# Optimization experiments

Hardware: AMD Instinct MI355X
Metric: run time of the kernel (lower is better)

The kernel has to match this reference:

```python
import jax, jax.numpy as jnp
import numpy as np

N_WIRES = 6
DIM = 1 << N_WIRES  # 64, equals input channel dim C for amplitude encoding
HID = N_WIRES       # hidden_dim = len(ops)


def _rx(theta):
    c = jnp.cos(theta / 2).astype(jnp.complex64)
    s = jnp.sin(theta / 2).astype(jnp.complex64)
    return jnp.stack([jnp.stack([c, -1j * s]), jnp.stack([-1j * s, c])])


def _ry(theta):
    c = jnp.cos(theta / 2).astype(jnp.complex64)
    s = jnp.sin(theta / 2).astype(jnp.complex64)
    return jnp.stack([jnp.stack([c, -s]), jnp.stack([s, c])])


def _apply_1q(state, U, wire):
    # state: (N, 2, 2, ..., 2); apply 2x2 U on qubit axis wire+1
    s = jnp.moveaxis(state, wire + 1, 1)
    s = jnp.einsum('ab,nb...->na...', U, s)
    return jnp.moveaxis(s, 1, wire + 1)


def _apply_cnot(state, c, t):
    # flip target axis where control bit == 1
    s = jnp.moveaxis(state, (c + 1, t + 1), (1, 2))
    s = jnp.concatenate([s[:, :1], jnp.flip(s[:, 1:2], axis=2)], axis=1)
    return jnp.moveaxis(s, (1, 2), (c + 1, t + 1))


def _expval_z(state, wire):
    # <Z_wire> = P(bit=0) - P(bit=1)
    p = state.real ** 2 + state.imag ** 2
    p = jnp.moveaxis(p, wire + 1, 1).reshape(p.shape[0], 2, -1)
    return p[:, 0].sum(-1) - p[:, 1].sum(-1)


def _value_layer(x_flat, params, qk):
    # amplitude encoding: normalize input into state amplitudes (C == DIM)
    norm = jnp.linalg.norm(x_flat, axis=-1, keepdims=True)
    psi = (x_flat / norm).astype(jnp.complex64)
    state = psi.reshape((x_flat.shape[0],) + (2,) * N_WIRES)
    rx0, ry0, ry1 = params[0], params[1], params[2]
    for j in range(N_WIRES):
        state = _apply_1q(state, _rx(rx0[j]), j)
        state = _apply_1q(state, _ry(ry0[j]), j)
    for j in range(N_WIRES):
        state = _apply_cnot(state, j, (j + 1) % N_WIRES)
    for j in range(N_WIRES):
        state = _apply_1q(state, _ry(ry1[j]), j)
    if qk:
        z0 = _expval_z(state, 0)
        return jnp.stack([z0] * HID, axis=-1)  # qk=True replicates wire-0 <Z>
    return jnp.stack([_expval_z(state, w) for w in range(N_WIRES)], axis=-1)


def setup_inputs() -> dict:
    key = jax.random.key(0)
    k1, k2, k3, k4 = jax.random.split(key, 4)
    B, T, C = 16, 2048, DIM
    return {
        'x': jax.random.normal(k1, (B, T, C), dtype=jnp.float32),
        'params_q': jax.random.normal(k2, (3, N_WIRES), dtype=jnp.float32),
        'params_k': jax.random.normal(k3, (3, N_WIRES), dtype=jnp.float32),
        'params_v': jax.random.normal(k4, (3, N_WIRES), dtype=jnp.float32),
    }


def reference(x, params_q, params_k, params_v):
    B, T, C = x.shape
    xf = x.reshape(B * T, C)
    q = _value_layer(xf, params_q, True).reshape(B, T, HID)
    k = _value_layer(xf, params_k, True).reshape(B, T, HID)
    v = _value_layer(xf, params_v, False).reshape(B, T, HID)
    scores = jnp.einsum('btd,bsd->bts', q, k) / jnp.sqrt(jnp.float32(HID))
    attn = jax.nn.softmax(scores, axis=-1)
    return jnp.einsum('bts,bsd->btd', attn, v)
```

## Files before the change

### kernel.cpp

```cpp
#include <hip/hip_runtime.h>
#include <math.h>

#define NWIRES 6
#define DIM 64
#define NTOK 32768
#define NBATCH 16
#define TPB 2048
#define NMOM 16
#define SQRT6F 2.4494897427831781f
#define APAD 76

typedef short bf16x8 __attribute__((ext_vector_type(8)));
typedef float f32x4  __attribute__((ext_vector_type(4)));

__device__ __forceinline__ unsigned f2bfbits(float f) {
    unsigned u = __float_as_uint(f);
    return (u + 0x7FFF + ((u >> 16) & 1)) >> 16;
}
__device__ __forceinline__ float bfbits2f(unsigned b) {
    return __uint_as_float(b << 16);
}

__global__ __launch_bounds__(128) void qsa_build(
        const float* __restrict__ pq,
        const float* __restrict__ pk,
        const float* __restrict__ pv,
        unsigned short* __restrict__ gA) {
    __shared__ float sTc[64], sTs[64], sP[24];
    int circ = blockIdx.x;
    const float* p = (circ == 0) ? pq : (circ == 1 ? pk : pv);
    int tid = threadIdx.x;

    if (tid < 64) {
        int b = tid;
        float d = 0.f;
#pragma unroll
        for (int j = 0; j < 6; ++j)
            d += 0.5f * p[j] * ((b & (32 >> j)) ? -1.f : 1.f);
        float sd, cd;
        sincosf(d, &sd, &cd);
        sTc[b] = cd;
        sTs[b] = sd;
        if (b < 12) {
            float s, cc;
            sincosf(0.5f * p[6 + b], &s, &cc);
            sP[b * 2 + 0] = cc;
            sP[b * 2 + 1] = s;
        }
    }
    __syncthreads();

    int ph = tid >> 6;
    int k  = tid & 63;
    const float* sTx = ph ? sTs : sTc;
    float v[64];
#pragma unroll
    for (int g = 0; g < 64; ++g)
        v[g] = (__popc(g & k) & 1) ? -sTx[g] : sTx[g];

#pragma unroll
    for (int M = 32; M >= 1; M >>= 1) {
#pragma unroll
        for (int i = 0; i < 64; ++i) {
            if (i & M) continue;
            int j = i | M;
            float a = v[i], b = v[j];
            v[i] = a + b; v[j] = a - b;
        }
    }

#pragma unroll
    for (int layer = 0; layer < 2; ++layer) {
        const float* Pl = sP + layer * 12;
#pragma unroll
        for (int w = 0; w < 6; ++w) {
            int M = 32 >> w;
            float c = Pl[w * 2], s = Pl[w * 2 + 1];
#pragma unroll
            for (int i = 0; i < 64; ++i) {
                if (i & M) continue;
                int j = i | M;
                float a = v[i], b = v[j];
                v[i] = c * a - s * b;
                v[j] = s * a + c * b;
            }
        }
        if (layer == 0) {
#pragma unroll
            for (int i = 32; i < 64; ++i) {
                if (i & 16) continue;
                int j = i | 16;
                float t = v[i]; v[i] = v[j]; v[j] = t;
            }
#pragma unroll
            for (int w = 1; w < 5; ++w) {
                int MC = 32 >> w, MT = MC >> 1;
#pragma unroll
                for (int i = 0; i < 64; ++i) {
                    if (!(i & MC) || (i & MT)) continue;
                    int j = i | MT;
                    float t = v[i]; v[i] = v[j]; v[j] = t;
                }
            }
#pragma unroll
            for (int i = 1; i < 32; i += 2) {
                int j = i | 32;
                float t = v[i]; v[i] = v[j]; v[j] = t;
            }
        }
    }

    unsigned short* g0 = gA + (size_t)circ * (2 * 128 * APAD);
#pragma unroll
    for (int i = 0; i < 64; ++i) {
        int row = ph * 64 + i;
        unsigned hb = f2bfbits(v[i]);
        unsigned lb = f2bfbits(v[i] - bfbits2f(hb));
        g0[row * APAD + k] = (unsigned short)hb;
        g0[128 * APAD + row * APAD + k] = (unsigned short)lb;
    }
}

__global__ __attribute__((amdgpu_waves_per_eu(1, 4)))
__launch_bounds__(256) void qsa_sim(
        const float* __restrict__ x,
        const unsigned short* __restrict__ gA,
        float* __restrict__ zq,
        float* __restrict__ kv) {
    __shared__ __align__(16) unsigned short sA[2 * 128 * APAD];
    unsigned short* sAh = sA;
    unsigned short* sAl = sA + 128 * APAD;
    int tid = threadIdx.x;
    int tbase = blockIdx.x * 128;
    int circ = blockIdx.y;

    int lane = tid & 63, wv = tid >> 6;
    int q4 = lane >> 4, c16 = lane & 15;
    int mytok0 = wv * 32 + c16;
    const float* xr0 = x + ((size_t)(tbase + mytok0)) * 64;
    float4 rw[4];
#pragma unroll
    for (int ks = 0; ks < 2; ++ks) {
        rw[ks * 2 + 0] = *(const float4*)(xr0 + ks * 32 + q4 * 8);
        rw[ks * 2 + 1] = *(const float4*)(xr0 + ks * 32 + q4 * 8 + 4);
    }

    {
        const uint4* gsrc = (const uint4*)(gA + (size_t)circ * (2 * 128 * APAD));
        uint4* ldst = (uint4*)sA;
#pragma unroll
        for (int c = 0; c < 9; ++c)
            ldst[tid + c * 256] = gsrc[tid + c * 256];
        if (tid < 128) ldst[tid + 9 * 256] = gsrc[tid + 9 * 256];
    }
    __syncthreads();

    bf16x8 xh[2], xl[2];
#pragma unroll 1
    for (int cg = 0; cg < 2; ++cg) {
#pragma unroll
        for (int ks = 0; ks < 2; ++ks) {
            float4 f0 = rw[ks * 2], f1 = rw[ks * 2 + 1];
            float ff[8] = {f0.x, f0.y, f0.z, f0.w, f1.x, f1.y, f1.z, f1.w};
#pragma unroll
            for (int e = 0; e < 8; ++e) {
                unsigned hb = f2bfbits(ff[e]);
                unsigned lb = f2bfbits(ff[e] - bfbits2f(hb));
                xh[ks][e] = (short)hb;
                xl[ks][e] = (short)lb;
            }
        }
        int mytok = wv * 32 + cg * 16 + c16;
        if (cg < 1) {
            const float* xrn = x + ((size_t)(tbase + mytok + 16)) * 64;
#pragma unroll
            for (int ks = 0; ks < 2; ++ks) {
                rw[ks * 2 + 0] = *(const float4*)(xrn + ks * 32 + q4 * 8);
                rw[ks * 2 + 1] = *(const float4*)(xrn + ks * 32 + q4 * 8 + 4);
            }
        }

        f32x4 acc[8];
#pragma unroll
        for (int mt = 0; mt < 8; ++mt) acc[mt] = (f32x4){0.f, 0.f, 0.f, 0.f};
#pragma unroll
        for (int mt = 0; mt < 8; ++mt) {
            int r = mt * 16 + c16;
#pragma unroll
            for (int ks = 0; ks < 2; ++ks) {
                const uint2* ph_ = (const uint2*)(&sAh[r * APAD + ks * 32 + q4 * 8]);
                const uint2* pl_ = (const uint2*)(&sAl[r * APAD + ks * 32 + q4 * 8]);
                union { uint2 u[2]; bf16x8 v; } ua, ub;
                ua.u[0] = ph_[0]; ua.u[1] = ph_[1];
                ub.u[0] = pl_[0]; ub.u[1] = pl_[1];
                bf16x8 ah = ua.v, al = ub.v;
                acc[mt] = __builtin_amdgcn_mfma_f32_16x16x32_bf16(ah, xh[ks], acc[mt], 0, 0, 0);
                acc[mt] = __builtin_amdgcn_mfma_f32_16x16x32_bf16(ah, xl[ks], acc[mt], 0, 0, 0);
                acc[mt] = __builtin_amdgcn_mfma_f32_16x16x32_bf16(al, xh[ks], acc[mt], 0, 0, 0);
            }
        }

        float n = 0.f, s0 = 0.f, s1 = 0.f, s2 = 0.f, s3 = 0.f, s4 = 0.f, s5 = 0.f;
        float f2 = (q4 < 2) ? 1.f : 0.f;
        float f3 = (q4 & 1) ? 0.f : 1.f;
#pragma unroll
        for (int mt = 0; mt < 4; ++mt) {
#pragma unroll
            for (int rg = 0; rg < 4; ++rg) {
                float dc = acc[mt][rg];
                float ds = acc[mt + 4][rg];
                float pp = dc * dc + ds * ds;
                n += pp;
                if (!(mt & 2)) s0 += pp;
                if (!(mt & 1)) s1 += pp;
                s2 += f2 * pp;
                s3 += f3 * pp;
                if (!(rg & 2)) s4 += pp;
                if (!(rg & 1)) s5 += pp;
            }
        }
#pragma unroll
        for (int d = 16; d <= 32; d <<= 1) {
            n  += __shfl_xor(n,  d, 64);
            s0 += __shfl_xor(s0, d, 64);
            s1 += __shfl_xor(s1, d, 64);
            s2 += __shfl_xor(s2, d, 64);
            s3 += __shfl_xor(s3, d, 64);
            s4 += __shfl_xor(s4, d, 64);
            s5 += __shfl_xor(s5, d, 64);
        }
        if (q4 == 0) {
            int t = tbase + mytok;
            float inv = 1.0f / n;
            if (circ == 0) {
                zq[t] = SQRT6F * (2.f * s0 - n) * inv;
            } else if (circ == 1) {
                kv[(size_t)t * 8] = (2.f * s0 - n) * inv;
            } else {
                float* o = kv + (size_t)t * 8;
                o[1] = (2.f*s0 - n) * inv;
                o[2] = (2.f*s1 - n) * inv;
                o[3] = (2.f*s2 - n) * inv;
                o[4] = (2.f*s3 - n) * inv;
                o[5] = (2.f*s4 - n) * inv;
                o[6] = (2.f*s5 - n) * inv;
                o[7] = 0.f;
            }
        }
    }
}

__global__ __attribute__((amdgpu_waves_per_eu(1, 2)))
__launch_bounds__(64) void qsa_moments_partial(
        const float* __restrict__ kv,
        float* __restrict__ mpart) {
    int blk = blockIdx.x;
    int b = blk >> 3, c = blk & 7;
    int lane = threadIdx.x;
    float S[NMOM], H[NMOM][6];
#pragma unroll
    for (int m = 0; m < NMOM; ++m) {
        S[m] = 0.f;
#pragma unroll
        for (int w = 0; w < 6; ++w) H[m][w] = 0.f;
    }
    const float* base = kv + ((size_t)(b * TPB + c * 256)) * 8;
#pragma unroll
    for (int r = 0; r < 4; ++r) {
        const float4* e = (const float4*)(base + (size_t)(r * 64 + lane) * 8);
        float4 e0 = e[0], e1 = e[1];
        float z = e0.x;
        float v0 = e0.y, v1 = e0.z, v2 = e0.w, v3 = e1.x, v4 = e1.y, v5 = e1.z;
        float pw = 1.f;
#pragma unroll
        for (int m = 0; m < NMOM; ++m) {
            S[m] += pw;
            H[m][0] += pw * v0; H[m][1] += pw * v1; H[m][2] += pw * v2;
            H[m][3] += pw * v3; H[m][4] += pw * v4; H[m][5] += pw * v5;
            pw *= z;
        }
    }
#pragma unroll
    for (int d = 32; d >= 1; d >>= 1) {
#pragma unroll
        for (int m = 0; m < NMOM; ++m) {
            S[m] += __shfl_xor(S[m], d, 64);
#pragma unroll
            for (int w = 0; w < 6; ++w) H[m][w] += __shfl_xor(H[m][w], d, 64);
        }
    }
    if (lane == 0) {
        float* o = mpart + (size_t)blk * 112;
#pragma unroll
        for (int m = 0; m < NMOM; ++m) {
            float* om = o + m * 7;
            om[0] = S[m];
            om[1] = H[m][0]; om[2] = H[m][1]; om[3] = H[m][2];
            om[4] = H[m][3]; om[5] = H[m][4]; om[6] = H[m][5];
        }
    }
}

__global__ __launch_bounds__(256) void qsa_eval(
        const float* __restrict__ zq,
        const float* __restrict__ mpart,
        float* __restrict__ out) {
    __shared__ float sm[112];
    int bk = blockIdx.x;
    int b = bk >> 3;
    int tid = threadIdx.x;
    if (tid < 112) {
        float s = 0.f;
#pragma unroll
        for (int c = 0; c < 8; ++c) s += mpart[(size_t)(b * 8 + c) * 112 + tid];
        sm[tid] = s;
    }
    __syncthreads();

    int t = bk * 256 + tid;
    float a = zq[t];
    float den = 0.f, o0 = 0.f, o1 = 0.f, o2 = 0.f, o3 = 0.f, o4 = 0.f, o5 = 0.f;
    float pw = 1.f;
#pragma unroll
    for (int m = 0; m < NMOM; ++m) {
        const float* mm = sm + m * 7;
        den += pw * mm[0];
        o0 += pw * mm[1]; o1 += pw * mm[2]; o2 += pw * mm[3];
        o3 += pw * mm[4]; o4 += pw * mm[5]; o5 += pw * mm[6];
        pw *= a * (1.0f / (m + 1));
    }
    float inv = 1.0f / den;
    float* o = out + (size_t)t * 6;
    float2* o2p = (float2*)o;
    o2p[0] = make_float2(o0 * inv, o1 * inv);
    o2p[1] = make_float2(o2 * inv, o3 * inv);
    o2p[2] = make_float2(o4 * inv, o5 * inv);
}

extern "C" void kernel_launch(void* const* d_in, const int* in_sizes, int n_in,
                              void* d_out, int out_size, void* d_ws, size_t ws_size,
                              hipStream_t stream) {
    const float* x  = (const float*)d_in[0];
    const float* pq = (const float*)d_in[1];
    const float* pk = (const float*)d_in[2];
    const float* pv = (const float*)d_in[3];
    float* w = (float*)d_ws;
    float* zq    = w;
    float* kv    = zq + NTOK;
    float* mpart = kv + NTOK * 8;
    unsigned short* gA = (unsigned short*)(mpart + NBATCH * 8 * 112);
    float* out   = (float*)d_out;

    qsa_build<<<3, 128, 0, stream>>>(pq, pk, pv, gA);
    qsa_sim<<<dim3(NTOK / 128, 3), 256, 0, stream>>>(x, gA, zq, kv);
    qsa_moments_partial<<<NBATCH * 8, 64, 0, stream>>>(kv, mpart);
    qsa_eval<<<NTOK / 256, 256, 0, stream>>>(zq, mpart, out);
}
```

Before: 87.76 us.

## Fuse moment accumulation into sim kernel and pre-swizzle circuit matrix into MFMA fragments

The circuit matrices are now stored in MFMA fragment order so each lane loads its A operand straight from global memory (L2-cached) with one 16-byte load, which removes the LDS staging copy and its barrier. The K and V circuits are computed in the same block, and the per-block power moments are reduced in shared memory and written out directly. This drops the kv intermediate buffer and the separate moments kernel. The grid changes from 256x3 blocks of 128 tokens to 512x2 blocks of 64 tokens, and the eval kernel now sums 32 partials per batch instead of 8, at the cost of repeated global A loads per wave and serial K then V work in one block.

```diff
diff --git a/kernel.cpp b/kernel.cpp
--- a/kernel.cpp
+++ b/kernel.cpp
@@ -8,7 +8,8 @@
 #define TPB 2048
 #define NMOM 16
 #define SQRT6F 2.4494897427831781f
-#define APAD 76
+#define FRAG 512
+#define CSTRIDE 16384
 
 typedef short bf16x8 __attribute__((ext_vector_type(8)));
 typedef float f32x4  __attribute__((ext_vector_type(4)));
@@ -110,14 +111,18 @@
         }
     }
 
-    unsigned short* g0 = gA + (size_t)circ * (2 * 128 * APAD);
+    unsigned short* g0 = gA + (size_t)circ * CSTRIDE;
+    int ks = k >> 5, q4 = (k >> 3) & 3, e = k & 7;
 #pragma unroll
     for (int i = 0; i < 64; ++i) {
-        int row = ph * 64 + i;
+        int r = ph * 64 + i;
+        int mt = r >> 4, c16 = r & 15;
+        int l = q4 * 16 + c16;
+        int off = ((mt * 2 + ks) << 9) + l * 8 + e;
         unsigned hb = f2bfbits(v[i]);
         unsigned lb = f2bfbits(v[i] - bfbits2f(hb));
-        g0[row * APAD + k] = (unsigned short)hb;
-        g0[128 * APAD + row * APAD + k] = (unsigned short)lb;
+        g0[off] = (unsigned short)hb;
+        g0[8192 + off] = (unsigned short)lb;
     }
 }
 
@@ -126,77 +131,62 @@
         const float* __restrict__ x,
         const unsigned short* __restrict__ gA,
         float* __restrict__ zq,
-        float* __restrict__ kv) {
-    __shared__ __align__(16) unsigned short sA[2 * 128 * APAD];
-    unsigned short* sAh = sA;
-    unsigned short* sAl = sA + 128 * APAD;
+        float* __restrict__ mpart) {
+    __shared__ float zT[64];
+    __shared__ __align__(16) float vT[6 * 68];
+    __shared__ __align__(16) float zpow[16 * 68];
     int tid = threadIdx.x;
-    int tbase = blockIdx.x * 128;
+    int bx = blockIdx.x;
     int circ = blockIdx.y;
+    int tbase = bx * 64;
 
     int lane = tid & 63, wv = tid >> 6;
     int q4 = lane >> 4, c16 = lane & 15;
-    int mytok0 = wv * 32 + c16;
-    const float* xr0 = x + ((size_t)(tbase + mytok0)) * 64;
+
+    const float* xr = x + ((size_t)(tbase + wv * 16 + c16)) * 64;
     float4 rw[4];
 #pragma unroll
     for (int ks = 0; ks < 2; ++ks) {
-        rw[ks * 2 + 0] = *(const float4*)(xr0 + ks * 32 + q4 * 8);
-        rw[ks * 2 + 1] = *(const float4*)(xr0 + ks * 32 + q4 * 8 + 4);
-    }
-
-    {
-        const uint4* gsrc = (const uint4*)(gA + (size_t)circ * (2 * 128 * APAD));
-        uint4* ldst = (uint4*)sA;
-#pragma unroll
-        for (int c = 0; c < 9; ++c)
-            ldst[tid + c * 256] = gsrc[tid + c * 256];
-        if (tid < 128) ldst[tid + 9 * 256] = gsrc[tid + 9 * 256];
-    }
-    __syncthreads();
+        rw[ks * 2 + 0] = *(const float4*)(xr + ks * 32 + q4 * 8);
+        rw[ks * 2 + 1] = *(const float4*)(xr + ks * 32 + q4 * 8 + 4);
+    }
 
     bf16x8 xh[2], xl[2];
+#pragma unroll
+    for (int ks = 0; ks < 2; ++ks) {
+        float4 f0 = rw[ks * 2], f1 = rw[ks * 2 + 1];
+        float ff[8] = {f0.x, f0.y, f0.z, f0.w, f1.x, f1.y, f1.z, f1.w};
+#pragma unroll
+        for (int e = 0; e < 8; ++e) {
+            unsigned hb = f2bfbits(ff[e]);
+            unsigned lb = f2bfbits(ff[e] - bfbits2f(hb));
+            xh[ks][e] = (short)hb;
+            xl[ks][e] = (short)lb;
+        }
+    }
+
+    int cc0 = circ ? 1 : 0;
+    int nc  = circ ? 2 : 1;
 #pragma unroll 1
-    for (int cg = 0; cg < 2; ++cg) {
-#pragma unroll
-        for (int ks = 0; ks < 2; ++ks) {
-            float4 f0 = rw[ks * 2], f1 = rw[ks * 2 + 1];
-            float ff[8] = {f0.x, f0.y, f0.z, f0.w, f1.x, f1.y, f1.z, f1.w};
-#pragma unroll
-            for (int e = 0; e < 8; ++e) {
-                unsigned hb = f2bfbits(ff[e]);
-                unsigned lb = f2bfbits(ff[e] - bfbits2f(hb));
-                xh[ks][e] = (short)hb;
-                xl[ks][e] = (short)lb;
-            }
-        }
-        int mytok = wv * 32 + cg * 16 + c16;
-        if (cg < 1) {
-            const float* xrn = x + ((size_t)(tbase + mytok + 16)) * 64;
+    for (int ci = 0; ci < nc; ++ci) {
+        int cc = cc0 + ci;
+        const unsigned short* Af = gA + (size_t)cc * CSTRIDE;
+
+        f32x4 acc[8];
+#pragma unroll
+        for (int mt = 0; mt < 8; ++mt) acc[mt] = (f32x4){0.f, 0.f, 0.f, 0.f};
+
+#pragma unroll
+        for (int mt = 0; mt < 8; ++mt) {
 #pragma unroll
             for (int ks = 0; ks < 2; ++ks) {
-                rw[ks * 2 + 0] = *(const float4*)(xrn + ks * 32 + q4 * 8);
-                rw[ks * 2 + 1] = *(const float4*)(xrn + ks * 32 + q4 * 8 + 4);
-            }
-        }
-
-        f32x4 acc[8];
-#pragma unroll
-        for (int mt = 0; mt < 8; ++mt) acc[mt] = (f32x4){0.f, 0.f, 0.f, 0.f};
-#pragma unroll
-        for (int mt = 0; mt < 8; ++mt) {
-            int r = mt * 16 + c16;
-#pragma unroll
-            for (int ks = 0; ks < 2; ++ks) {
-                const uint2* ph_ = (const uint2*)(&sAh[r * APAD + ks * 32 + q4 * 8]);
-                const uint2* pl_ = (const uint2*)(&sAl[r * APAD + ks * 32 + q4 * 8]);
-                union { uint2 u[2]; bf16x8 v; } ua, ub;
-                ua.u[0] = ph_[0]; ua.u[1] = ph_[1];
-                ub.u[0] = pl_[0]; ub.u[1] = pl_[1];
-                bf16x8 ah = ua.v, al = ub.v;
-                acc[mt] = __builtin_amdgcn_mfma_f32_16x16x32_bf16(ah, xh[ks], acc[mt], 0, 0, 0);
-                acc[mt] = __builtin_amdgcn_mfma_f32_16x16x32_bf16(ah, xl[ks], acc[mt], 0, 0, 0);
-                acc[mt] = __builtin_amdgcn_mfma_f32_16x16x32_bf16(al, xh[ks], acc[mt], 0, 0, 0);
+                int off = ((mt * 2 + ks) << 9) + lane * 8;
+                union { uint4 u; bf16x8 v; } ua, ub;
+                ua.u = *(const uint4*)(Af + off);
+                ub.u = *(const uint4*)(Af + 8192 + off);
+                acc[mt] = __builtin_amdgcn_mfma_f32_16x16x32_bf16(ua.v, xh[ks], acc[mt], 0, 0, 0);
+                acc[mt] = __builtin_amdgcn_mfma_f32_16x16x32_bf16(ua.v, xl[ks], acc[mt], 0, 0, 0);
+                acc[mt] = __builtin_amdgcn_mfma_f32_16x16x32_bf16(ub.v, xh[ks], acc[mt], 0, 0, 0);
             }
         }
 
@@ -230,73 +220,52 @@
             s5 += __shfl_xor(s5, d, 64);
         }
         if (q4 == 0) {
-            int t = tbase + mytok;
+            int tl = wv * 16 + c16;
             float inv = 1.0f / n;
             if (circ == 0) {
-                zq[t] = SQRT6F * (2.f * s0 - n) * inv;
-            } else if (circ == 1) {
-                kv[(size_t)t * 8] = (2.f * s0 - n) * inv;
+                zq[tbase + tl] = SQRT6F * (2.f * s0 - n) * inv;
+            } else if (cc == 1) {
+                zT[tl] = (2.f * s0 - n) * inv;
             } else {
-                float* o = kv + (size_t)t * 8;
-                o[1] = (2.f*s0 - n) * inv;
-                o[2] = (2.f*s1 - n) * inv;
-                o[3] = (2.f*s2 - n) * inv;
-                o[4] = (2.f*s3 - n) * inv;
-                o[5] = (2.f*s4 - n) * inv;
-                o[6] = (2.f*s5 - n) * inv;
-                o[7] = 0.f;
-            }
-        }
-    }
-}
-
-__global__ __attribute__((amdgpu_waves_per_eu(1, 2)))
-__launch_bounds__(64) void qsa_moments_partial(
-        const float* __restrict__ kv,
-        float* __restrict__ mpart) {
-    int blk = blockIdx.x;
-    int b = blk >> 3, c = blk & 7;
-    int lane = threadIdx.x;
-    float S[NMOM], H[NMOM][6];
-#pragma unroll
-    for (int m = 0; m < NMOM; ++m) {
-        S[m] = 0.f;
-#pragma unroll
-        for (int w = 0; w < 6; ++w) H[m][w] = 0.f;
-    }
-    const float* base = kv + ((size_t)(b * TPB + c * 256)) * 8;
-#pragma unroll
-    for (int r = 0; r < 4; ++r) {
-        const float4* e = (const float4*)(base + (size_t)(r * 64 + lane) * 8);
-        float4 e0 = e[0], e1 = e[1];
-        float z = e0.x;
-        float v0 = e0.y, v1 = e0.z, v2 = e0.w, v3 = e1.x, v4 = e1.y, v5 = e1.z;
-        float pw = 1.f;
-#pragma unroll
-        for (int m = 0; m < NMOM; ++m) {
-            S[m] += pw;
-            H[m][0] += pw * v0; H[m][1] += pw * v1; H[m][2] += pw * v2;
-            H[m][3] += pw * v3; H[m][4] += pw * v4; H[m][5] += pw * v5;
-            pw *= z;
-        }
-    }
-#pragma unroll
-    for (int d = 32; d >= 1; d >>= 1) {
-#pragma unroll
-        for (int m = 0; m < NMOM; ++m) {
-            S[m] += __shfl_xor(S[m], d, 64);
-#pragma unroll
-            for (int w = 0; w < 6; ++w) H[m][w] += __shfl_xor(H[m][w], d, 64);
-        }
-    }
-    if (lane == 0) {
-        float* o = mpart + (size_t)blk * 112;
-#pragma unroll
-        for (int m = 0; m < NMOM; ++m) {
-            float* om = o + m * 7;
-            om[0] = S[m];
-            om[1] = H[m][0]; om[2] = H[m][1]; om[3] = H[m][2];
-            om[4] = H[m][3]; om[5] = H[m][4]; om[6] = H[m][5];
+                vT[0 * 68 + tl] = (2.f * s0 - n) * inv;
+                vT[1 * 68 + tl] = (2.f * s1 - n) * inv;
+                vT[2 * 68 + tl] = (2.f * s2 - n) * inv;
+                vT[3 * 68 + tl] = (2.f * s3 - n) * inv;
+                vT[4 * 68 + tl] = (2.f * s4 - n) * inv;
+                vT[5 * 68 + tl] = (2.f * s5 - n) * inv;
+            }
+        }
+    }
+
+    if (circ == 1) {
+        __syncthreads();
+        if (tid < 64) {
+            float z = zT[tid];
+            float pw = 1.f;
+#pragma unroll
+            for (int m = 0; m < NMOM; ++m) { zpow[m * 68 + tid] = pw; pw *= z; }
+        }
+        __syncthreads();
+        if (tid < 112) {
+            int m = tid / 7, w = tid - m * 7;
+            const float4* zp = (const float4*)&zpow[m * 68];
+            float a = 0.f;
+            if (w == 6) {
+#pragma unroll
+                for (int k = 0; k < 16; ++k) {
+                    float4 a4 = zp[k];
+                    a += a4.x + a4.y + a4.z + a4.w;
+                }
+            } else {
+                const float4* vp = (const float4*)&vT[w * 68];
+#pragma unroll
+                for (int k = 0; k < 16; ++k) {
+                    float4 a4 = zp[k], b4 = vp[k];
+                    a += a4.x * b4.x + a4.y * b4.y + a4.z * b4.z + a4.w * b4.w;
+                }
+            }
+            int idx = m * 7 + ((w == 6) ? 0 : (w + 1));
+            mpart[(size_t)bx * 112 + idx] = a;
         }
     }
 }
@@ -312,7 +281,7 @@
     if (tid < 112) {
         float s = 0.f;
 #pragma unroll
-        for (int c = 0; c < 8; ++c) s += mpart[(size_t)(b * 8 + c) * 112 + tid];
+        for (int c = 0; c < 32; ++c) s += mpart[(size_t)(b * 32 + c) * 112 + tid];
         sm[tid] = s;
     }
     __syncthreads();
@@ -346,13 +315,11 @@
     const float* pv = (const float*)d_in[3];
     float* w = (float*)d_ws;
     float* zq    = w;
-    float* kv    = zq + NTOK;
-    float* mpart = kv + NTOK * 8;
-    unsigned short* gA = (unsigned short*)(mpart + NBATCH * 8 * 112);
+    float* mpart = zq + NTOK;
+    unsigned short* gA = (unsigned short*)(mpart + 512 * 112);
     float* out   = (float*)d_out;
 
     qsa_build<<<3, 128, 0, stream>>>(pq, pk, pv, gA);
-    qsa_sim<<<dim3(NTOK / 128, 3), 256, 0, stream>>>(x, gA, zq, kv);
-    qsa_moments_partial<<<NBATCH * 8, 64, 0, stream>>>(kv, mpart);
+    qsa_sim<<<dim3(512, 2), 256, 0, stream>>>(x, gA, zq, mpart);
     qsa_eval<<<NTOK / 256, 256, 0, stream>>>(zq, mpart, out);
 }
```

Result: faster. 83.35 us (-5.0%).
